# Kernel tuning notes

Measured on AMD Instinct MI355X. Metric: run time of the kernel, lower is better.

## Reference

```python
import jax, jax.numpy as jnp
import numpy as np

TOP_K = 2
NUM_EXPERTS = 8


def setup_inputs() -> dict:
    key = jax.random.key(0)
    ks = jax.random.split(key, 8)
    h, d, ds, E = 1024, 512, 1024, NUM_EXPERTS
    s = 1.0 / np.sqrt(h)
    return {
        "x": jax.random.normal(ks[0], (2, 2048, h), jnp.float32),
        "router": jax.random.normal(ks[1], (h, E), jnp.float32) * s,
        "experts_gate": jax.random.normal(ks[2], (E, h, d), jnp.float32) * s,
        "experts_up": jax.random.normal(ks[3], (E, h, d), jnp.float32) * s,
        "experts_down": jax.random.normal(ks[4], (E, d, h), jnp.float32) * (1.0 / np.sqrt(d)),
        "shared_gate": jax.random.normal(ks[5], (h, ds), jnp.float32) * s,
        "shared_up": jax.random.normal(ks[6], (h, ds), jnp.float32) * s,
        "shared_down": jax.random.normal(ks[7], (ds, h), jnp.float32) * (1.0 / np.sqrt(ds)),
    }


def reference(x, router, experts_gate, experts_up, experts_down,
              shared_gate, shared_up, shared_down):
    b, s, h = x.shape
    E = router.shape[1]
    # Shared expert path (SwiGLU)
    shared_act = jax.nn.silu(jnp.einsum('bsh,hd->bsd', x, shared_gate))
    shared_up_out = jnp.einsum('bsh,hd->bsd', x, shared_up)
    shared_out = jnp.einsum('bsd,dh->bsh', shared_act * shared_up_out, shared_down)
    # Router: softmax over experts, top-k selection
    router_probs = jax.nn.softmax(jnp.einsum('bsh,he->bse', x, router), axis=-1)
    topk_probs, topk_idx = jax.lax.top_k(router_probs, TOP_K)  # [b,s,k]
    # Dense per-token expert coefficient matrix: coef[t,e] = prob if expert e selected else 0
    coef = jnp.sum(jax.nn.one_hot(topk_idx, E, dtype=x.dtype) * topk_probs[..., None], axis=2)
    coef = coef.reshape(b * s, E)  # [T,E]
    x_flat = x.reshape(b * s, h)
    # Grouped expert SwiGLU (mathematically identical to gather->gemm->scatter_add;
    # unrouted token contributions are zeroed by coef)
    gate = jnp.einsum('th,ehd->etd', x_flat, experts_gate)
    up = jnp.einsum('th,ehd->etd', x_flat, experts_up)
    expert_out = jnp.einsum('etd,edh->eth', jax.nn.silu(gate) * up, experts_down)
    routed = jnp.einsum('eth,te->th', expert_out, coef)
    return routed.reshape(b, s, h) + shared_out
```

## Files before the change

kernel.cpp:

```cpp
#include <hip/hip_runtime.h>
#include <hip/hip_bf16.h>
#include <stdint.h>

typedef short bf16x8 __attribute__((ext_vector_type(8)));
typedef float f32x4 __attribute__((ext_vector_type(4)));
typedef unsigned short u16;

#define GLOAD16(gp, lp)                                                        \
  __builtin_amdgcn_global_load_lds(                                            \
      (const __attribute__((address_space(1))) void*)(gp),                     \
      (__attribute__((address_space(3))) void*)(lp), 16, 0, 0)

__device__ __forceinline__ u16 f2bf(float f) {
  uint32_t u = __builtin_bit_cast(uint32_t, f);
  u = (u + 0x7FFFu + ((u >> 16) & 1u)) >> 16;
  return (u16)u;
}
__device__ __forceinline__ float bf2f(u16 v) {
  return __builtin_bit_cast(float, (uint32_t)v << 16);
}

__device__ __forceinline__ int swzoff(int row, int u) {
  int p = row >> 1;
  int us = ((row & 1) * 4 + u) ^ (p & 7);
  return p * 128 + us * 16;
}

__global__ void mega(const float* __restrict__ x, const float* __restrict__ rw,
                     const float* __restrict__ eg, const float* __restrict__ eu,
                     const float* __restrict__ ed, const float* __restrict__ sg,
                     const float* __restrict__ su, const float* __restrict__ sd,
                     u16* __restrict__ Xb, u16* __restrict__ WpT,
                     u16* __restrict__ WdT, float4* __restrict__ meta) {
  __shared__ float t[64][65];
  const int tid = threadIdx.x;
  const int b = blockIdx.x;
  if (b < 1280) {
    const float* src; int kbase, kt, ht;
    if (b < 1024) { src = ed; kbase = 0;    kt = b >> 4;          ht = b & 15; }
    else          { src = sd; kbase = 4096; kt = (b - 1024) >> 4; ht = b & 15; }
    const int k0 = kt * 64, h0 = ht * 64;
#pragma unroll
    for (int p = 0; p < 4; ++p) {
      int r = p * 16 + (tid >> 4), c = (tid & 15) * 4;
      float4 v = *(const float4*)&src[(size_t)(k0 + r) * 1024 + h0 + c];
      t[r][c] = v.x; t[r][c + 1] = v.y; t[r][c + 2] = v.z; t[r][c + 3] = v.w;
    }
    __syncthreads();
#pragma unroll
    for (int p = 0; p < 4; ++p) {
      int hl = p * 16 + (tid >> 4), kl = (tid & 15) * 4;
      ushort4 o;
      o.x = f2bf(t[kl][hl]);     o.y = f2bf(t[kl + 1][hl]);
      o.z = f2bf(t[kl + 2][hl]); o.w = f2bf(t[kl + 3][hl]);
      *(ushort4*)&WdT[(size_t)(h0 + hl) * 5120 + kbase + k0 + kl] = o;
    }
  } else if (b < 3840) {
    int bb = b - 1280;
    const float* src; int pbase, C, dt, ht;
    if (bb < 2048) {
      int slice = bb >> 7, r = bb & 127;
      int e = slice >> 1; int up = slice & 1;
      src = (up ? eu : eg) + (size_t)e * 524288;
      pbase = e * 1024 + up * 32; C = 512;
      dt = r >> 4; ht = r & 15;
    } else {
      int r = bb - 2048;
      int up = r >= 256; r &= 255;
      src = up ? su : sg; pbase = 8192 + up * 32; C = 1024;
      dt = r >> 4; ht = r & 15;
    }
    const int d0 = dt * 64, h0 = ht * 64;
#pragma unroll
    for (int p = 0; p < 4; ++p) {
      int hl = p * 16 + (tid >> 4), dl = (tid & 15) * 4;
      float4 v = *(const float4*)&src[(size_t)(h0 + hl) * C + d0 + dl];
      t[hl][dl] = v.x; t[hl][dl + 1] = v.y; t[hl][dl + 2] = v.z; t[hl][dl + 3] = v.w;
    }
    __syncthreads();
#pragma unroll
    for (int p = 0; p < 4; ++p) {
      int dl = p * 16 + (tid >> 4), hl = (tid & 15) * 4;
      int d = d0 + dl;
      int prow = pbase + ((d >> 5) << 6) + (d & 31);
      ushort4 o;
      o.x = f2bf(t[hl][dl]);     o.y = f2bf(t[hl + 1][dl]);
      o.z = f2bf(t[hl + 2][dl]); o.w = f2bf(t[hl + 3][dl]);
      *(ushort4*)&WpT[(size_t)prow * 1024 + h0 + hl] = o;
    }
  } else if (b < 4864) {
    const int l = tid & 63;
    const int tok = (b - 3840) * 4 + (tid >> 6);
    const float* xr = x + (size_t)tok * 1024;
    float acc[8];
#pragma unroll
    for (int e = 0; e < 8; ++e) acc[e] = 0.f;
    for (int it = 0; it < 16; ++it) {
      int h = it * 64 + l;
      float xv = xr[h];
      float4 r0 = *(const float4*)&rw[h * 8];
      float4 r1 = *(const float4*)&rw[h * 8 + 4];
      acc[0] += xv * r0.x; acc[1] += xv * r0.y; acc[2] += xv * r0.z; acc[3] += xv * r0.w;
      acc[4] += xv * r1.x; acc[5] += xv * r1.y; acc[6] += xv * r1.z; acc[7] += xv * r1.w;
    }
#pragma unroll
    for (int off = 32; off >= 1; off >>= 1) {
#pragma unroll
      for (int e = 0; e < 8; ++e) acc[e] += __shfl_xor(acc[e], off, 64);
    }
    if (l == 0) {
      float m = acc[0];
#pragma unroll
      for (int e = 1; e < 8; ++e) m = fmaxf(m, acc[e]);
      float p[8], s = 0.f;
#pragma unroll
      for (int e = 0; e < 8; ++e) { p[e] = expf(acc[e] - m); s += p[e]; }
      int i1 = 0;
#pragma unroll
      for (int e = 1; e < 8; ++e) if (p[e] > p[i1]) i1 = e;
      int i2 = (i1 == 0) ? 1 : 0;
#pragma unroll
      for (int e = 0; e < 8; ++e) if (e != i1 && p[e] > p[i2]) i2 = e;
      float inv = 1.f / s;
      meta[tok] = make_float4(__int_as_float(i1), __int_as_float(i2),
                              p[i1] * inv, p[i2] * inv);
    }
  } else {
    int i = (b - 4864) * 512 + tid;
#pragma unroll
    for (int k = 0; k < 2; ++k) {
      float4 v = ((const float4*)x)[i + k * 256];
      ushort4 o;
      o.x = f2bf(v.x); o.y = f2bf(v.y); o.z = f2bf(v.z); o.w = f2bf(v.w);
      ((ushort4*)Xb)[i + k * 256] = o;
    }
  }
}

__global__ __launch_bounds__(512) void assign_k(const float4* __restrict__ meta,
                                                int* __restrict__ counts_g,
                                                int* __restrict__ list_tok,
                                                int2* __restrict__ t2s) {
  __shared__ int cnt_s[8];
  const int E = threadIdx.x >> 6;
  const int lane = threadIdx.x & 63;
  const unsigned long long lt = (lane == 63) ? ~0ull >> 1 : ((1ull << lane) - 1ull) | 0ull;

  int total = 0;
#pragma unroll 8
  for (int it = 0; it < 64; ++it) {
    float4 m = meta[it * 64 + lane];
    bool sel = (__float_as_int(m.x) == E) || (__float_as_int(m.y) == E);
    total += __popcll(__ballot(sel));
  }
  if (lane == 0) { cnt_s[E] = total; counts_g[E] = total; }
  __syncthreads();
  int base = 0;
#pragma unroll
  for (int e = 0; e < 8; ++e) base += (e < E) ? cnt_s[e] : 0;

  int running = base;
  for (int it = 0; it < 64; ++it) {
    int tok = it * 64 + lane;
    float4 m = meta[tok];
    bool s1 = (__float_as_int(m.x) == E);
    bool s2 = (__float_as_int(m.y) == E);
    unsigned long long mask = __ballot(s1 || s2);
    int pos = running + __popcll(mask & lt);
    if (s1 || s2) {
      list_tok[pos] = tok;
      if (s1) t2s[tok].x = pos;
      else    t2s[tok].y = pos;
    }
    running += __popcll(mask);
  }
}

template <int MODE>
__global__ __launch_bounds__(512, 2) void moe_gemm(
    const u16* __restrict__ Xb, const u16* __restrict__ WpT,
    const u16* __restrict__ WdT, u16* __restrict__ Hs,
    u16* __restrict__ Hcomp, u16* __restrict__ Pb, float* __restrict__ out,
    const int* __restrict__ counts, const int* __restrict__ list_tok) {
  constexpr int SLOT = (128 + 256) * 64;
  constexpr int BOFF = 128 * 64;
  __shared__ __align__(16) char lds[3 * SLOT];

  const int tid = threadIdx.x;
  const int l = tid & 63, l15 = l & 15, lg = l >> 4;
  const int wv = tid >> 6, wr = wv >> 2, wc = wv & 3;

  const int id = blockIdx.x;
  const bool routed = id < 288;
  int expert = 0, m0 = 0, n0 = 0, base = 0, count = 0, nt;

  if (routed) {
    int mtf = id >> 2; n0 = (id & 3) * 256;
    int acc_ = 0, bas = 0, found = 0;
#pragma unroll
    for (int e = 0; e < 8; ++e) {
      int c = counts[e];
      int nm = (c + 127) >> 7;
      if (!found && mtf < acc_ + nm) {
        expert = e; m0 = (mtf - acc_) * 128; base = bas; count = c; found = 1;
      }
      acc_ += nm; bas += c;
    }
    if (!found) return;
  } else {
    int sid = id - 288;
    if (MODE == 0) { m0 = (sid >> 3) * 128; n0 = (sid & 7) * 256; }
    else           { m0 = (sid >> 2) * 128; n0 = (sid & 3) * 256; }
  }
  nt = (MODE == 1 && routed) ? 16 : 32;

  const char* gA0; const char* gB[2]; int lA0, lB[2];
  {
    int L = tid * 16;
    int p = L >> 7, uph = (L >> 4) & 7;
    int usw = uph ^ (p & 7);
    int row = 2 * p + (usw >> 2), ulog = usw & 3;
    const u16* ap;
    if (MODE == 0) {
      if (routed) {
        int ar = min(m0 + row, count - 1);
        ap = Xb + (size_t)list_tok[base + ar] * 1024;
      } else ap = Xb + (size_t)(m0 + row) * 1024;
    } else {
      if (routed) ap = Hcomp + (size_t)(base + m0 + row) * 512;
      else        ap = Hs + (size_t)(m0 + row) * 1024;
    }
    gA0 = (const char*)ap + ulog * 16;
    lA0 = L;
  }
#pragma unroll
  for (int j = 0; j < 2; ++j) {
    int L = (j * 512 + tid) * 16;
    int p = L >> 7, uph = (L >> 4) & 7;
    int usw = uph ^ (p & 7);
    int row = 2 * p + (usw >> 2), ulog = usw & 3;
    const u16* bp;
    if (MODE == 0) {
      int rbase = routed ? expert * 1024 : 8192;
      bp = WpT + (size_t)(rbase + n0 + row) * 1024;
    } else {
      int kb = routed ? expert * 512 : 4096;
      bp = WdT + (size_t)(n0 + row) * 5120 + kb;
    }
    gB[j] = (const char*)bp + ulog * 16;
    lB[j] = L;
  }

  int offA[4], offB[4];
#pragma unroll
  for (int m = 0; m < 4; ++m) offA[m] = swzoff(wr * 64 + m * 16 + l15, lg);
#pragma unroll
  for (int n = 0; n < 4; ++n) offB[n] = BOFF + swzoff(wc * 64 + n * 16 + l15, lg);

  f32x4 acc[4][4];
#pragma unroll
  for (int m = 0; m < 4; ++m)
#pragma unroll
    for (int n = 0; n < 4; ++n) acc[m][n] = {0.f, 0.f, 0.f, 0.f};

#define STAGE(T)                                                               \
  {                                                                            \
    char* sb_ = lds + (((T) % 3) * SLOT);                                      \
    const int tb_ = (T) * 64;                                                  \
    GLOAD16(gA0 + tb_, sb_ + lA0);                                             \
    GLOAD16(gB[0] + tb_, sb_ + BOFF + lB[0]);                                  \
    GLOAD16(gB[1] + tb_, sb_ + BOFF + lB[1]);                                  \
  }

  STAGE(0); STAGE(1);
  asm volatile("s_waitcnt vmcnt(3)" ::: "memory");
  __builtin_amdgcn_s_barrier();

  for (int t = 0; t < nt; ++t) {
    asm volatile("" ::: "memory");
    char* sb = lds + ((t % 3) * SLOT);
    bf16x8 af[4], bfr[4];
#pragma unroll
    for (int m = 0; m < 4; ++m) af[m] = *(const bf16x8*)(sb + offA[m]);
#pragma unroll
    for (int n = 0; n < 4; ++n) bfr[n] = *(const bf16x8*)(sb + offB[n]);
    if (t + 2 < nt) {
      STAGE(t + 2);
      asm volatile("s_waitcnt vmcnt(3)" ::: "memory");
    } else if (t + 2 == nt) {
      asm volatile("s_waitcnt vmcnt(0)" ::: "memory");
    }
    __builtin_amdgcn_s_barrier();
    __builtin_amdgcn_s_setprio(1);
#pragma unroll
    for (int m = 0; m < 4; ++m)
#pragma unroll
      for (int n = 0; n < 4; ++n)
        acc[m][n] = __builtin_amdgcn_mfma_f32_16x16x32_bf16(af[m], bfr[n], acc[m][n], 0, 0, 0);
    __builtin_amdgcn_s_setprio(0);
    asm volatile("" ::: "memory");
    __builtin_amdgcn_s_barrier();
  }
#undef STAGE

  const int rbl = wr * 64 + lg * 4;
  const int cnt_lim = routed ? count : (1 << 30);
  if constexpr (MODE == 0) {
    u16* dst = routed ? Hcomp : Hs;
    const int ldH = routed ? 512 : 1024;
    const int rowbase = routed ? (base + m0) : m0;
    const int cD0 = (n0 + wc * 64) >> 1;
#pragma unroll
    for (int m = 0; m < 4; ++m)
#pragma unroll
      for (int q = 0; q < 2; ++q) {
        int cD = cD0 + q * 16 + l15;
#pragma unroll
        for (int j = 0; j < 4; ++j) {
          int mrow = rbl + m * 16 + j;
          if (m0 + mrow < cnt_lim) {
            float g = acc[m][q][j];
            float u = acc[m][q + 2][j];
            dst[(size_t)(rowbase + mrow) * ldH + cD] =
                f2bf(g / (1.f + __expf(-g)) * u);
          }
        }
      }
  } else {
    const int cb = n0 + wc * 64;
#pragma unroll
    for (int m = 0; m < 4; ++m)
#pragma unroll
      for (int n = 0; n < 4; ++n)
#pragma unroll
        for (int j = 0; j < 4; ++j) {
          int mrow = rbl + m * 16 + j;
          if (m0 + mrow < cnt_lim) {
            int col = cb + n * 16 + l15;
            if (routed)
              Pb[(size_t)(base + m0 + mrow) * 1024 + col] = f2bf(acc[m][n][j]);
            else
              out[(size_t)(m0 + mrow) * 1024 + col] = acc[m][n][j];
          }
        }
  }
}

__global__ void reduce_k(const float4* __restrict__ meta, const int2* __restrict__ t2s,
                         const u16* __restrict__ Pb, float* __restrict__ out) {
  const int t = blockIdx.x;
  const int c = threadIdx.x * 4;
  float4 m = meta[t];
  int2 s = t2s[t];
  float p1 = m.z, p2 = m.w;
  ushort4 a = *(const ushort4*)&Pb[(size_t)s.x * 1024 + c];
  ushort4 bb = *(const ushort4*)&Pb[(size_t)s.y * 1024 + c];
  float4 o = *(float4*)&out[(size_t)t * 1024 + c];
  o.x += p1 * bf2f(a.x) + p2 * bf2f(bb.x);
  o.y += p1 * bf2f(a.y) + p2 * bf2f(bb.y);
  o.z += p1 * bf2f(a.z) + p2 * bf2f(bb.z);
  o.w += p1 * bf2f(a.w) + p2 * bf2f(bb.w);
  *(float4*)&out[(size_t)t * 1024 + c] = o;
}

extern "C" void kernel_launch(void* const* d_in, const int* in_sizes, int n_in,
                              void* d_out, int out_size, void* d_ws, size_t ws_size,
                              hipStream_t stream) {
  const float* x  = (const float*)d_in[0];
  const float* rw = (const float*)d_in[1];
  const float* eg = (const float*)d_in[2];
  const float* eu = (const float*)d_in[3];
  const float* ed = (const float*)d_in[4];
  const float* sg = (const float*)d_in[5];
  const float* su = (const float*)d_in[6];
  const float* sd = (const float*)d_in[7];
  float* out = (float*)d_out;

  char* ws = (char*)d_ws;
  u16*    Xb    = (u16*)(ws);
  u16*    WpT   = (u16*)(ws + 8388608);
  u16*    WdT   = (u16*)(ws + 29360128);
  u16*    Hs    = (u16*)(ws + 39845888);
  u16*    Hcomp = (u16*)(ws + 48234496);
  u16*    Pb    = (u16*)(ws + 56623104);
  float4* meta  = (float4*)(ws + 73400320);
  int2*   t2s   = (int2*)(ws + 73465856);
  int*    counts= (int*)(ws + 73498624);
  int*    list_tok = (int*)(ws + 73498688);

  mega<<<6912, 256, 0, stream>>>(x, rw, eg, eu, ed, sg, su, sd,
                                 Xb, WpT, WdT, meta);
  assign_k<<<1, 512, 0, stream>>>(meta, counts, list_tok, t2s);

  moe_gemm<0><<<544, 512, 0, stream>>>(Xb, WpT, WdT, Hs, Hcomp, Pb, out,
                                       counts, list_tok);
  moe_gemm<1><<<416, 512, 0, stream>>>(Xb, WpT, WdT, Hs, Hcomp, Pb, out,
                                       counts, list_tok);

  reduce_k<<<4096, 256, 0, stream>>>(meta, t2s, Pb, out);
}
```

Baseline: 141.7 us.

## Double-buffer GEMM LDS for three blocks per CU and cache routing meta in LDS

The GEMM pipeline moves from a three-slot to a two-slot LDS ring and raises the launch bound to three blocks per CU, trading prefetch depth for occupancy. The load/wait/barrier order is rearranged so the next tile is issued before computing on the current one. The assign kernel now packs the top-k expert ids into a shared u16 array once, instead of every wave rereading meta from global memory twice. The down-projection A pointer is also clamped to the expert's count, which avoids reading past the end of the group.

```diff
diff --git a/kernel.cpp b/kernel.cpp
--- a/kernel.cpp
+++ b/kernel.cpp
@@ -141,17 +141,25 @@
                                                 int* __restrict__ counts_g,
                                                 int* __restrict__ list_tok,
                                                 int2* __restrict__ t2s) {
+  __shared__ u16 sel[4096];
   __shared__ int cnt_s[8];
-  const int E = threadIdx.x >> 6;
-  const int lane = threadIdx.x & 63;
-  const unsigned long long lt = (lane == 63) ? ~0ull >> 1 : ((1ull << lane) - 1ull) | 0ull;
+  const int tid = threadIdx.x;
+  for (int i = tid; i < 4096; i += 512) {
+    float4 m = meta[i];
+    sel[i] = (u16)(__float_as_int(m.x) | (__float_as_int(m.y) << 8));
+  }
+  __syncthreads();
+
+  const int E = tid >> 6;
+  const int lane = tid & 63;
+  const unsigned long long lt = (lane == 63) ? ~0ull >> 1 : ((1ull << lane) - 1ull);
 
   int total = 0;
 #pragma unroll 8
   for (int it = 0; it < 64; ++it) {
-    float4 m = meta[it * 64 + lane];
-    bool sel = (__float_as_int(m.x) == E) || (__float_as_int(m.y) == E);
-    total += __popcll(__ballot(sel));
+    u16 s = sel[it * 64 + lane];
+    bool any = ((s & 255) == E) || ((s >> 8) == E);
+    total += __popcll(__ballot(any));
   }
   if (lane == 0) { cnt_s[E] = total; counts_g[E] = total; }
   __syncthreads();
@@ -162,9 +170,9 @@
   int running = base;
   for (int it = 0; it < 64; ++it) {
     int tok = it * 64 + lane;
-    float4 m = meta[tok];
-    bool s1 = (__float_as_int(m.x) == E);
-    bool s2 = (__float_as_int(m.y) == E);
+    u16 s = sel[tok];
+    bool s1 = ((s & 255) == E);
+    bool s2 = ((s >> 8) == E);
     unsigned long long mask = __ballot(s1 || s2);
     int pos = running + __popcll(mask & lt);
     if (s1 || s2) {
@@ -177,14 +185,14 @@
 }
 
 template <int MODE>
-__global__ __launch_bounds__(512, 2) void moe_gemm(
+__global__ __launch_bounds__(512, 3) void moe_gemm(
     const u16* __restrict__ Xb, const u16* __restrict__ WpT,
     const u16* __restrict__ WdT, u16* __restrict__ Hs,
     u16* __restrict__ Hcomp, u16* __restrict__ Pb, float* __restrict__ out,
     const int* __restrict__ counts, const int* __restrict__ list_tok) {
   constexpr int SLOT = (128 + 256) * 64;
   constexpr int BOFF = 128 * 64;
-  __shared__ __align__(16) char lds[3 * SLOT];
+  __shared__ __align__(16) char lds[2 * SLOT];
 
   const int tid = threadIdx.x;
   const int l = tid & 63, l15 = l & 15, lg = l >> 4;
@@ -227,7 +235,7 @@
         ap = Xb + (size_t)list_tok[base + ar] * 1024;
       } else ap = Xb + (size_t)(m0 + row) * 1024;
     } else {
-      if (routed) ap = Hcomp + (size_t)(base + m0 + row) * 512;
+      if (routed) ap = Hcomp + (size_t)(base + min(m0 + row, count - 1)) * 512;
       else        ap = Hs + (size_t)(m0 + row) * 1024;
     }
     gA0 = (const char*)ap + ulog * 16;
@@ -265,32 +273,30 @@
 
 #define STAGE(T)                                                               \
   {                                                                            \
-    char* sb_ = lds + (((T) % 3) * SLOT);                                      \
+    char* sb_ = lds + (((T) & 1) * SLOT);                                      \
     const int tb_ = (T) * 64;                                                  \
     GLOAD16(gA0 + tb_, sb_ + lA0);                                             \
     GLOAD16(gB[0] + tb_, sb_ + BOFF + lB[0]);                                  \
     GLOAD16(gB[1] + tb_, sb_ + BOFF + lB[1]);                                  \
   }
 
-  STAGE(0); STAGE(1);
-  asm volatile("s_waitcnt vmcnt(3)" ::: "memory");
-  __builtin_amdgcn_s_barrier();
+  STAGE(0);
 
   for (int t = 0; t < nt; ++t) {
+    if (t + 1 < nt) {
+      STAGE(t + 1);
+      asm volatile("s_waitcnt vmcnt(3)" ::: "memory");
+    } else {
+      asm volatile("s_waitcnt vmcnt(0)" ::: "memory");
+    }
+    __builtin_amdgcn_s_barrier();
     asm volatile("" ::: "memory");
-    char* sb = lds + ((t % 3) * SLOT);
+    char* sb = lds + ((t & 1) * SLOT);
     bf16x8 af[4], bfr[4];
 #pragma unroll
     for (int m = 0; m < 4; ++m) af[m] = *(const bf16x8*)(sb + offA[m]);
 #pragma unroll
     for (int n = 0; n < 4; ++n) bfr[n] = *(const bf16x8*)(sb + offB[n]);
-    if (t + 2 < nt) {
-      STAGE(t + 2);
-      asm volatile("s_waitcnt vmcnt(3)" ::: "memory");
-    } else if (t + 2 == nt) {
-      asm volatile("s_waitcnt vmcnt(0)" ::: "memory");
-    }
-    __builtin_amdgcn_s_barrier();
     __builtin_amdgcn_s_setprio(1);
 #pragma unroll
     for (int m = 0; m < 4; ++m)
```

Result: faster. 130.3 us (-8.0%).
